# Kernel optimization log

Measured on AMD Instinct MI355X. Metric: run time of the kernel, lower is better.

## Reference

```python
import jax, jax.numpy as jnp
import numpy as np

HEADS = 4

def _rope(Q, K):
    # Q, K: [B, T, H, F]; split last dim into 4 chunks of w = F // 4
    w = Q.shape[-1] // 4
    T = Q.shape[-3]
    Q1r, Q1i, Q2r, Q2i = jnp.split(Q, 4, axis=-1)
    K1r, K1i, K2r, K2i = jnp.split(K, 4, axis=-1)
    Pt = jnp.arange(T, dtype=Q.dtype).reshape(1, -1, 1, 1)
    Df = (2.0 ** (-jnp.arange(w, dtype=Q.dtype))).reshape(1, 1, 1, -1)
    U = Pt * Df / 16.0
    Ur, Ui = jnp.sin(U), jnp.cos(U)  # names match the original (sin first)
    rot = lambda r, i: (r * Ur - i * Ui, r * Ui + i * Ur)
    Q1r, Q1i = rot(Q1r, Q1i)
    Q2r, Q2i = rot(Q2r, Q2i)
    K1r, K1i = rot(K1r, K1i)
    K2r, K2i = rot(K2r, K2i)
    return (jnp.concatenate([Q1r, Q1i], -1), jnp.concatenate([Q2r, Q2i], -1),
            jnp.concatenate([K1r, K1i], -1), jnp.concatenate([K2r, K2i], -1))


def setup_inputs() -> dict:
    key = jax.random.key(0)
    ks = jax.random.split(key, 8)
    B, F, T = 4, 512, 2048
    sd = 1.0 / np.sqrt(F)
    return {
        "x": jax.random.normal(ks[0], (B, F, T), jnp.float32),
        "Wq": jax.random.normal(ks[1], (F, F), jnp.float32) * sd,
        "bq": jax.random.normal(ks[2], (F,), jnp.float32) * sd,
        "Wk": jax.random.normal(ks[3], (F, F), jnp.float32) * sd,
        "bk": jax.random.normal(ks[4], (F,), jnp.float32) * sd,
        "Wv": jax.random.normal(ks[5], (F, F), jnp.float32) * sd,
        "bv": jax.random.normal(ks[6], (F,), jnp.float32) * sd,
        "s2": jax.random.uniform(ks[7], (HEADS,), jnp.float32),
    }


def reference(x, Wq, bq, Wk, bk, Wv, bv, s2):
    # x: [B, feat, T] -> transpose to [B, T, feat]; cond defaults to x
    B, F, T = x.shape
    H = HEADS
    hf = F // H
    scale = jnp.asarray(np.sqrt(F // 2), x.dtype)
    xt = jnp.swapaxes(x, -1, -2)  # [B, T, F]
    Q = (xt @ Wq.T + bq).reshape(B, T, H, hf)
    K = (xt @ Wk.T + bk).reshape(B, T, H, hf)
    V = (xt @ Wv.T + bv).reshape(B, T, H, hf)
    Q1, Q2, K1, K2 = _rope(Q, K)
    A1 = jax.nn.softmax(jnp.einsum('bqhf,bkhf->bhqk', Q1, K1) / scale, axis=-1)
    A2 = jax.nn.softmax(jnp.einsum('bqhf,bkhf->bhqk', Q2, K2) / scale, axis=-1)
    A = A1 - A2 * s2[None, :, None, None]
    R = jnp.einsum('bhqk,bkhf->bqhf', A, V)
    y = R.reshape(B, T, F)
    return jnp.swapaxes(xt + y, -1, -2)  # [B, feat, T]
```

## Files before the change

### kernel.cpp

```cpp
#include <hip/hip_runtime.h>
#include <math.h>

#define B_DIM 4
#define F_DIM 512
#define T_DIM 2048
#define H_DIM 4
#define HF    128

typedef __attribute__((ext_vector_type(8))) short short8;
typedef __attribute__((ext_vector_type(4))) float floatx4;

__device__ __forceinline__ unsigned short f2bf(float f) {
    return (unsigned short)((__float_as_uint(f) + 0x8000u) >> 16);
}

__device__ __forceinline__ unsigned pkbf2(float a, float b) {
    const unsigned ua = __float_as_uint(a) + 0x8000u;
    const unsigned ub = __float_as_uint(b) + 0x8000u;
    return __builtin_amdgcn_perm(ub, ua, 0x07060302u);
}

__device__ __forceinline__ short8 pack8(const float* v) {
    union { unsigned u[4]; short8 s; } r;
    #pragma unroll
    for (int j = 0; j < 4; ++j) r.u[j] = pkbf2(v[2*j], v[2*j+1]);
    return r.s;
}

__device__ __forceinline__ void gload16(const unsigned short* g, unsigned short* l) {
    __builtin_amdgcn_global_load_lds(
        (const __attribute__((address_space(1))) void*)g,
        (__attribute__((address_space(3))) void*)l, 16, 0, 0);
}

__global__ __launch_bounds__(256)
void prep_kernel(const float* __restrict__ x,
                 const float* __restrict__ Wq, const float* __restrict__ Wk,
                 const float* __restrict__ Wv,
                 unsigned short* __restrict__ xt,
                 unsigned short* __restrict__ Wqb, unsigned short* __restrict__ Wkb,
                 unsigned short* __restrict__ Wvb)
{
    const int tid = threadIdx.x;
    if (blockIdx.z < B_DIM) {
        const int b  = blockIdx.z;
        const int t0 = blockIdx.x * 64;
        const int f0 = blockIdx.y * 64;
        __shared__ float Ls[64][67];
        const float* __restrict__ xb = x + (size_t)b * F_DIM * T_DIM;
        #pragma unroll
        for (int it = 0; it < 4; ++it) {
            const int fr = (tid >> 4) + 16 * it;
            const int tc = (tid & 15) << 2;
            const float4 v = *(const float4*)(xb + (size_t)(f0 + fr) * T_DIM + t0 + tc);
            Ls[fr][tc+0] = v.x; Ls[fr][tc+1] = v.y; Ls[fr][tc+2] = v.z; Ls[fr][tc+3] = v.w;
        }
        __syncthreads();
        const int f8 = tid & 7;
        const int tb = tid >> 3;
        #pragma unroll
        for (int it2 = 0; it2 < 2; ++it2) {
            const int t = tb + 32 * it2;
            float v[8];
            #pragma unroll
            for (int j = 0; j < 8; ++j) v[j] = Ls[8*f8 + j][t];
            *(short8*)(xt + ((size_t)b * T_DIM + t0 + t) * F_DIM + f0 + 8*f8) = pack8(v);
        }
    } else {
        const int blockId = blockIdx.y * 32 + blockIdx.x;
        const int g0 = blockId * 256 + tid;
        const int perW = F_DIM * F_DIM / 8;
        for (int chunk = g0; chunk < 3 * perW; chunk += 65536) {
            const int wsel = chunk / perW;
            const int rem  = chunk - wsel * perW;
            const float* __restrict__ Ws = (wsel == 0) ? Wq : (wsel == 1) ? Wk : Wv;
            unsigned short* __restrict__ Wd = (wsel == 0) ? Wqb : (wsel == 1) ? Wkb : Wvb;
            float v[8];
            *(float4*)&v[0] = *(const float4*)(Ws + (size_t)rem * 8);
            *(float4*)&v[4] = *(const float4*)(Ws + (size_t)rem * 8 + 4);
            *(short8*)(Wd + (size_t)rem * 8) = pack8(v);
        }
    }
}

#define ASTR 136

__global__ __launch_bounds__(256, 3)
void proj_kernel(const unsigned short* __restrict__ xt,
                 const unsigned short* __restrict__ Wqb,
                 const unsigned short* __restrict__ Wkb,
                 const unsigned short* __restrict__ Wvb,
                 const float* __restrict__ bq, const float* __restrict__ bk,
                 const float* __restrict__ bv,
                 unsigned short* __restrict__ Qb, unsigned short* __restrict__ Kb,
                 unsigned short* __restrict__ Vtb)
{
    __shared__ unsigned short As[128][ASTR];
    __shared__ unsigned short Bs[64][ASTR];

    const int tid  = threadIdx.x;
    const int w    = tid >> 6;
    const int lane = tid & 63;
    const int ln15 = lane & 15;
    const int quad = lane >> 4;

    const bool is_v = (blockIdx.z >= 8);
    int t0, fo0, b;
    const unsigned short *Asrc, *Bsrc;
    if (!is_v) {
        t0  = blockIdx.x * 128;
        fo0 = blockIdx.y * 64;
        b   = blockIdx.z >> 1;
        Asrc = xt + (size_t)b * T_DIM * F_DIM + (size_t)t0 * F_DIM;
        Bsrc = ((blockIdx.z & 1) ? Wkb : Wqb) + (size_t)fo0 * F_DIM;
    } else {
        const int idx = blockIdx.y * 16 + blockIdx.x;
        fo0 = (idx >> 5) * 128;
        t0  = (idx & 31) * 64;
        b   = blockIdx.z - 8;
        Asrc = Wvb + (size_t)fo0 * F_DIM;
        Bsrc = xt + (size_t)b * T_DIM * F_DIM + (size_t)t0 * F_DIM;
    }

    floatx4 acc[2][4];
    #pragma unroll
    for (int mi = 0; mi < 2; ++mi)
        #pragma unroll
        for (int nt = 0; nt < 4; ++nt) acc[mi][nt] = (floatx4){0.f,0.f,0.f,0.f};

    for (int f0 = 0; f0 < F_DIM; f0 += 128) {
        __syncthreads();
        #pragma unroll
        for (int it = 0; it < 8; ++it) {
            const int idx = tid + it * 256;
            const int r = idx >> 4, c = (idx & 15) * 8;
            *(short8*)&As[r][c] = *(const short8*)(Asrc + (size_t)r * F_DIM + f0 + c);
        }
        #pragma unroll
        for (int it = 0; it < 4; ++it) {
            const int idx = tid + it * 256;
            const int r = idx >> 4, c = (idx & 15) * 8;
            *(short8*)&Bs[r][c] = *(const short8*)(Bsrc + (size_t)r * F_DIM + f0 + c);
        }
        __syncthreads();
        #pragma unroll
        for (int ks = 0; ks < 4; ++ks) {
            short8 a[2], bb[4];
            a[0] = *(const short8*)&As[w*32      + ln15][ks*32 + quad*8];
            a[1] = *(const short8*)&As[w*32 + 16 + ln15][ks*32 + quad*8];
            #pragma unroll
            for (int nt = 0; nt < 4; ++nt)
                bb[nt] = *(const short8*)&Bs[16*nt + ln15][ks*32 + quad*8];
            #pragma unroll
            for (int mi = 0; mi < 2; ++mi)
                #pragma unroll
                for (int nt = 0; nt < 4; ++nt)
                    acc[mi][nt] = __builtin_amdgcn_mfma_f32_16x16x32_bf16(
                        a[mi], bb[nt], acc[mi][nt], 0, 0, 0);
        }
    }

    if (!is_v) {
        const int which = blockIdx.z & 1;
        const float* bias = which ? bk : bq;
        unsigned short* __restrict__ Out =
            (which ? Kb : Qb) + (size_t)b * T_DIM * F_DIM;
        const float oscale = which ? 1.0f : 0.0625f * 1.4426950408889634f;
        float bn[4];
        #pragma unroll
        for (int nt = 0; nt < 4; ++nt) bn[nt] = bias[fo0 + 16*nt + ln15];
        const float pw[2] = {
            __uint_as_float((unsigned)(123 - ln15) << 23),
            __uint_as_float((unsigned)(107 - ln15) << 23)
        };
        #pragma unroll
        for (int mi = 0; mi < 2; ++mi) {
            #pragma unroll
            for (int r = 0; r < 4; ++r) {
                const int t = t0 + w*32 + 16*mi + quad*4 + r;
                unsigned short* rowp = Out + (size_t)t * F_DIM + fo0;
                #pragma unroll
                for (int pr = 0; pr < 2; ++pr) {
                    const int wi = 16*pr + ln15;
                    const float re = acc[mi][pr  ][r] + bn[pr];
                    const float im = acc[mi][pr+2][r] + bn[pr+2];
                    const float u = (float)t * pw[pr];
                    float sn, cs;
                    __sincosf(u, &sn, &cs);
                    rowp[wi]      = f2bf((re * sn - im * cs) * oscale);
                    rowp[wi + 32] = f2bf((re * cs + im * sn) * oscale);
                }
            }
        }
    } else {
        #pragma unroll
        for (int mi = 0; mi < 2; ++mi) {
            #pragma unroll
            for (int r = 0; r < 4; ++r) {
                const int fo = fo0 + w*32 + 16*mi + quad*4 + r;
                const float bvv = bv[fo];
                unsigned short* rowp = Vtb + ((size_t)b * F_DIM + fo) * T_DIM + t0;
                #pragma unroll
                for (int nt = 0; nt < 4; ++nt)
                    rowp[16*nt + ln15] = f2bf(acc[mi][nt][r] + bvv);
            }
        }
    }
}

__global__ __launch_bounds__(512, 2)
void attn_kernel(const unsigned short* __restrict__ Qb,
                 const unsigned short* __restrict__ Kb,
                 const unsigned short* __restrict__ Vtb,
                 const float* __restrict__ x,
                 const float* __restrict__ s2g,
                 float* __restrict__ out)
{
    __shared__ unsigned short smem[2][2][16384];

    const int tid  = threadIdx.x;
    const int w8   = tid >> 6;
    const int half = w8 >> 2;
    const int qg   = w8 & 3;
    const int lane = tid & 63;
    const int ln15 = lane & 15;
    const int quad = lane >> 4;

    const int flat = blockIdx.x + 16 * (blockIdx.y + 4 * blockIdx.z);
    const int swz  = (flat & 7) * 32 + (flat >> 3);
    const int q0 = (swz & 15) * 128;
    const int h  = (swz >> 4) & 3;
    const int b  = swz >> 6;

    const int kbase = half << 10;

    const unsigned short* __restrict__ Qg =
        Qb + ((size_t)b * T_DIM + q0 + qg * 32) * F_DIM + h * HF;
    const unsigned short* __restrict__ Kg =
        Kb + (size_t)b * T_DIM * F_DIM + h * HF;
    const unsigned short* __restrict__ Vg =
        Vtb + ((size_t)b * F_DIM + h * HF) * T_DIM;

    int koff[4], voff[4];
    #pragma unroll
    for (int it = 0; it < 4; ++it) {
        const int m = qg * 4 + it;
        {
            const int rd = 4 * m + (lane >> 4);
            const int r  = (rd & 32) | ((rd & 12) << 1) | ((rd & 16) >> 2) | (rd & 3);
            const int c  = (lane & 15) ^ (rd & 15);
            koff[it] = r * F_DIM + c * 8;
        }
        {
            const int rd = 8 * m + (lane >> 3);
            const int c  = (lane & 7) ^ (rd & 7);
            voff[it] = rd * T_DIM + c * 8;
        }
    }

    auto stage = [&](int buf, int k) {
        unsigned short* Kd = &smem[half][buf][0]    + qg * 2048;
        unsigned short* Vd = &smem[half][buf][8192] + qg * 2048;
        const unsigned short* Kp = Kg + (size_t)(kbase + k) * F_DIM;
        const unsigned short* Vp = Vg + (kbase + k);
        #pragma unroll
        for (int it = 0; it < 4; ++it) {
            gload16(Kp + koff[it], Kd + it * 512);
            gload16(Vp + voff[it], Vd + it * 512);
        }
    };

    short8 qa[2][4];
    #pragma unroll
    for (int g = 0; g < 2; ++g)
        #pragma unroll
        for (int c = 0; c < 4; ++c)
            qa[g][c] = *(const short8*)(Qg + (size_t)(g * 16 + ln15) * F_DIM + quad * 8 + 32 * c);

    floatx4 O1t[2][8], O2t[2][8];
    #pragma unroll
    for (int g = 0; g < 2; ++g)
        #pragma unroll
        for (int ft = 0; ft < 8; ++ft) {
            O1t[g][ft] = (floatx4){0.f, 0.f, 0.f, 0.f};
            O2t[g][ft] = (floatx4){0.f, 0.f, 0.f, 0.f};
        }
    float l1[2] = {0.f, 0.f}, l2[2] = {0.f, 0.f};

    stage(0, 0);

    for (int k0 = 0; k0 < 1024; k0 += 64) {
        asm volatile("s_waitcnt vmcnt(0)" ::: "memory");
        __syncthreads();
        const int buf = (k0 >> 6) & 1;
        if (k0 + 64 < 1024) stage(buf ^ 1, k0 + 64);

        const unsigned short* Ks = &smem[half][buf][0];
        const unsigned short* Vs = &smem[half][buf][8192];

        short8 p1f[2][2], p2f[2][2];
        #pragma unroll
        for (int tp = 0; tp < 2; ++tp) {
            float e1[2][8], e2[2][8];
            #pragma unroll
            for (int tt = 0; tt < 2; ++tt) {
                const int t = tp * 2 + tt;
                const unsigned short* krow = &Ks[(16 * t + ln15) * 128];
                const short8 k0f = *(const short8*)(krow + ((quad     ) ^ ln15) * 8);
                const short8 k1f = *(const short8*)(krow + ((quad +  4) ^ ln15) * 8);
                const short8 k2f = *(const short8*)(krow + ((quad +  8) ^ ln15) * 8);
                const short8 k3f = *(const short8*)(krow + ((quad + 12) ^ ln15) * 8);
                #pragma unroll
                for (int g = 0; g < 2; ++g) {
                    floatx4 z = (floatx4){0.f, 0.f, 0.f, 0.f};
                    floatx4 s = __builtin_amdgcn_mfma_f32_16x16x32_bf16(k0f, qa[g][0], z, 0, 0, 0);
                    s         = __builtin_amdgcn_mfma_f32_16x16x32_bf16(k1f, qa[g][1], s, 0, 0, 0);
                    floatx4 u = __builtin_amdgcn_mfma_f32_16x16x32_bf16(k2f, qa[g][2], z, 0, 0, 0);
                    u         = __builtin_amdgcn_mfma_f32_16x16x32_bf16(k3f, qa[g][3], u, 0, 0, 0);
                    #pragma unroll
                    for (int r = 0; r < 4; ++r) {
                        e1[g][tt*4 + r] = __builtin_amdgcn_exp2f(s[r]);
                        e2[g][tt*4 + r] = __builtin_amdgcn_exp2f(u[r]);
                    }
                }
            }
            #pragma unroll
            for (int g = 0; g < 2; ++g) {
                #pragma unroll
                for (int j = 0; j < 8; ++j) { l1[g] += e1[g][j]; l2[g] += e2[g][j]; }
                p1f[g][tp] = pack8(&e1[g][0]);
                p2f[g][tp] = pack8(&e2[g][0]);
            }
        }

        #pragma unroll
        for (int p = 0; p < 2; ++p) {
            #pragma unroll
            for (int ft = 0; ft < 8; ++ft) {
                const short8 va = *(const short8*)
                    (&Vs[(16*ft + ln15) * 64 + (((4*p + quad) ^ (ln15 & 7))) * 8]);
                O1t[0][ft] = __builtin_amdgcn_mfma_f32_16x16x32_bf16(va, p1f[0][p], O1t[0][ft], 0, 0, 0);
                O1t[1][ft] = __builtin_amdgcn_mfma_f32_16x16x32_bf16(va, p1f[1][p], O1t[1][ft], 0, 0, 0);
                O2t[0][ft] = __builtin_amdgcn_mfma_f32_16x16x32_bf16(va, p2f[0][p], O2t[0][ft], 0, 0, 0);
                O2t[1][ft] = __builtin_amdgcn_mfma_f32_16x16x32_bf16(va, p2f[1][p], O2t[1][ft], 0, 0, 0);
            }
        }
    }

    #pragma unroll
    for (int g = 0; g < 2; ++g) {
        l1[g] += __shfl_xor(l1[g], 16); l1[g] += __shfl_xor(l1[g], 32);
        l2[g] += __shfl_xor(l2[g], 16); l2[g] += __shfl_xor(l2[g], 32);
    }

    float* comb = (float*)&smem[0][0][0];
    __syncthreads();
    if (half == 1) {
        if (quad == 0) {
            #pragma unroll
            for (int g = 0; g < 2; ++g) {
                comb[      qg*32 + g*16 + ln15] = l1[g];
                comb[128 + qg*32 + g*16 + ln15] = l2[g];
            }
        }
        #pragma unroll
        for (int g = 0; g < 2; ++g)
            #pragma unroll
            for (int ft = 0; ft < 8; ++ft)
                #pragma unroll
                for (int r = 0; r < 4; ++r)
                    comb[512 + (((g*8 + ft)*4 + r) * 256) + qg*64 + lane] = O1t[g][ft][r];
    }
    __syncthreads();
    if (half == 0) {
        #pragma unroll
        for (int g = 0; g < 2; ++g) {
            l1[g] += comb[      qg*32 + g*16 + ln15];
            l2[g] += comb[128 + qg*32 + g*16 + ln15];
        }
        #pragma unroll
        for (int g = 0; g < 2; ++g)
            #pragma unroll
            for (int ft = 0; ft < 8; ++ft)
                #pragma unroll
                for (int r = 0; r < 4; ++r)
                    O1t[g][ft][r] += comb[512 + (((g*8 + ft)*4 + r) * 256) + qg*64 + lane];
    }
    __syncthreads();
    if (half == 1) {
        #pragma unroll
        for (int g = 0; g < 2; ++g)
            #pragma unroll
            for (int ft = 0; ft < 8; ++ft)
                #pragma unroll
                for (int r = 0; r < 4; ++r)
                    comb[512 + (((g*8 + ft)*4 + r) * 256) + qg*64 + lane] = O2t[g][ft][r];
    }
    __syncthreads();
    if (half == 0) {
        #pragma unroll
        for (int g = 0; g < 2; ++g)
            #pragma unroll
            for (int ft = 0; ft < 8; ++ft)
                #pragma unroll
                for (int r = 0; r < 4; ++r)
                    O2t[g][ft][r] += comb[512 + (((g*8 + ft)*4 + r) * 256) + qg*64 + lane];

        const float s2h = s2g[h];
        float i1[2], i2[2];
        #pragma unroll
        for (int g = 0; g < 2; ++g) { i1[g] = 1.f / l1[g]; i2[g] = s2h / l2[g]; }
        const size_t obase = (size_t)b * F_DIM * T_DIM;
        const int f0 = h * HF;
        #pragma unroll
        for (int g = 0; g < 2; ++g) {
            const int t = q0 + qg*32 + g*16 + ln15;
            #pragma unroll
            for (int ft = 0; ft < 8; ++ft) {
                #pragma unroll
                for (int r = 0; r < 4; ++r) {
                    const int feat = 16*ft + 4*quad + r;
                    const size_t idx = obase + (size_t)(f0 + feat) * T_DIM + t;
                    out[idx] = x[idx] + O1t[g][ft][r] * i1[g] - O2t[g][ft][r] * i2[g];
                }
            }
        }
    }
}

extern "C" void kernel_launch(void* const* d_in, const int* in_sizes, int n_in,
                              void* d_out, int out_size, void* d_ws, size_t ws_size,
                              hipStream_t stream)
{
    const float* x  = (const float*)d_in[0];
    const float* Wq = (const float*)d_in[1];
    const float* bq = (const float*)d_in[2];
    const float* Wk = (const float*)d_in[3];
    const float* bk = (const float*)d_in[4];
    const float* Wv = (const float*)d_in[5];
    const float* bv = (const float*)d_in[6];
    const float* s2 = (const float*)d_in[7];
    float* out = (float*)d_out;

    const size_t per = (size_t)B_DIM * T_DIM * F_DIM;
    const size_t wsz = (size_t)F_DIM * F_DIM;
    unsigned short* xt  = (unsigned short*)d_ws;
    unsigned short* Wqb = xt + per;
    unsigned short* Wkb = Wqb + wsz;
    unsigned short* Wvb = Wkb + wsz;
    unsigned short* Qb  = Wvb + wsz;
    unsigned short* Kb  = Qb + per;
    unsigned short* Vtb = Kb + per;

    hipLaunchKernelGGL(prep_kernel, dim3(32, 8, 5), dim3(256), 0, stream,
                       x, Wq, Wk, Wv, xt, Wqb, Wkb, Wvb);

    hipLaunchKernelGGL(proj_kernel, dim3(16, 8, 12), dim3(256), 0, stream,
                       xt, Wqb, Wkb, Wvb, bq, bk, bv, Qb, Kb, Vtb);

    hipLaunchKernelGGL(attn_kernel, dim3(16, 4, 4), dim3(512), 0, stream,
                       Qb, Kb, Vtb, x, s2, out);
}
```

Measured before the change: 93.31 us.

## Software-pipeline attention inner loop: interleave exp with PV MFMAs, add setprio

Restructures the attention main loop. The outer loop is unrolled by two so buffer offsets become compile-time constants, and LDS pointers are precomputed per lane. The QK MFMAs for the second key half and the exp/pack work are interleaved with the PV MFMAs so transcendental VALU work overlaps matrix work. s_setprio raises wave priority around the MFMA bursts. The interleaving adds register pressure from holding more score tiles live, which could reduce occupancy or cause spills.

```diff
diff --git a/kernel.cpp b/kernel.cpp
--- a/kernel.cpp
+++ b/kernel.cpp
@@ -258,92 +258,183 @@
         }
     }
 
-    auto stage = [&](int buf, int k) {
-        unsigned short* Kd = &smem[half][buf][0]    + qg * 2048;
-        unsigned short* Vd = &smem[half][buf][8192] + qg * 2048;
-        const unsigned short* Kp = Kg + (size_t)(kbase + k) * F_DIM;
-        const unsigned short* Vp = Vg + (kbase + k);
+    const unsigned short* kp[4];
+    #pragma unroll
+    for (int j = 0; j < 4; ++j)
+        kp[j] = &smem[half][0][0] + ln15 * 128 + ((quad + 4*j) ^ ln15) * 8;
+    const unsigned short* vp[2];
+    #pragma unroll
+    for (int p = 0; p < 2; ++p)
+        vp[p] = &smem[half][0][8192] + ln15 * 64 + (((4*p + quad) ^ (ln15 & 7))) * 8;
+
+    short8 qa[2][4];
+    #pragma unroll
+    for (int g = 0; g < 2; ++g)
+        #pragma unroll
+        for (int c = 0; c < 4; ++c)
+            qa[g][c] = *(const short8*)(Qg + (size_t)(g * 16 + ln15) * F_DIM + quad * 8 + 32 * c);
+
+    floatx4 O1t[2][8], O2t[2][8];
+    #pragma unroll
+    for (int g = 0; g < 2; ++g)
+        #pragma unroll
+        for (int ft = 0; ft < 8; ++ft) {
+            O1t[g][ft] = (floatx4){0.f, 0.f, 0.f, 0.f};
+            O2t[g][ft] = (floatx4){0.f, 0.f, 0.f, 0.f};
+        }
+    float l1[2] = {0.f, 0.f}, l2[2] = {0.f, 0.f};
+
+    {
+        unsigned short* Kd = &smem[half][0][0]    + qg * 2048;
+        unsigned short* Vd = &smem[half][0][8192] + qg * 2048;
+        const unsigned short* Kp = Kg + (size_t)kbase * F_DIM;
+        const unsigned short* Vp = Vg + kbase;
         #pragma unroll
         for (int it = 0; it < 4; ++it) {
             gload16(Kp + koff[it], Kd + it * 512);
             gload16(Vp + voff[it], Vd + it * 512);
         }
-    };
-
-    short8 qa[2][4];
-    #pragma unroll
-    for (int g = 0; g < 2; ++g)
-        #pragma unroll
-        for (int c = 0; c < 4; ++c)
-            qa[g][c] = *(const short8*)(Qg + (size_t)(g * 16 + ln15) * F_DIM + quad * 8 + 32 * c);
-
-    floatx4 O1t[2][8], O2t[2][8];
-    #pragma unroll
-    for (int g = 0; g < 2; ++g)
-        #pragma unroll
-        for (int ft = 0; ft < 8; ++ft) {
-            O1t[g][ft] = (floatx4){0.f, 0.f, 0.f, 0.f};
-            O2t[g][ft] = (floatx4){0.f, 0.f, 0.f, 0.f};
-        }
-    float l1[2] = {0.f, 0.f}, l2[2] = {0.f, 0.f};
-
-    stage(0, 0);
-
-    for (int k0 = 0; k0 < 1024; k0 += 64) {
-        asm volatile("s_waitcnt vmcnt(0)" ::: "memory");
-        __syncthreads();
-        const int buf = (k0 >> 6) & 1;
-        if (k0 + 64 < 1024) stage(buf ^ 1, k0 + 64);
-
-        const unsigned short* Ks = &smem[half][buf][0];
-        const unsigned short* Vs = &smem[half][buf][8192];
-
-        short8 p1f[2][2], p2f[2][2];
-        #pragma unroll
-        for (int tp = 0; tp < 2; ++tp) {
-            float e1[2][8], e2[2][8];
+    }
+
+    for (int k0o = 0; k0o < 1024; k0o += 128) {
+        #pragma unroll
+        for (int sub = 0; sub < 2; ++sub) {
+            const int k0 = k0o + sub * 64;
+            asm volatile("s_waitcnt vmcnt(0)" ::: "memory");
+            __syncthreads();
+
+            if (k0 + 64 < 1024) {
+                unsigned short* Kd = &smem[half][sub ^ 1][0]    + qg * 2048;
+                unsigned short* Vd = &smem[half][sub ^ 1][8192] + qg * 2048;
+                const unsigned short* Kp = Kg + (size_t)(kbase + k0 + 64) * F_DIM;
+                const unsigned short* Vp = Vg + (kbase + k0 + 64);
+                #pragma unroll
+                for (int it = 0; it < 4; ++it) {
+                    gload16(Kp + koff[it], Kd + it * 512);
+                    gload16(Vp + voff[it], Vd + it * 512);
+                }
+            }
+
+            const int BO = sub * 16384;
+
+            floatx4 sA[2][2], uA[2][2];
+            __builtin_amdgcn_s_setprio(1);
             #pragma unroll
             for (int tt = 0; tt < 2; ++tt) {
-                const int t = tp * 2 + tt;
-                const unsigned short* krow = &Ks[(16 * t + ln15) * 128];
-                const short8 k0f = *(const short8*)(krow + ((quad     ) ^ ln15) * 8);
-                const short8 k1f = *(const short8*)(krow + ((quad +  4) ^ ln15) * 8);
-                const short8 k2f = *(const short8*)(krow + ((quad +  8) ^ ln15) * 8);
-                const short8 k3f = *(const short8*)(krow + ((quad + 12) ^ ln15) * 8);
+                const short8 k0f = *(const short8*)(kp[0] + BO + tt * 2048);
+                const short8 k1f = *(const short8*)(kp[1] + BO + tt * 2048);
+                const short8 k2f = *(const short8*)(kp[2] + BO + tt * 2048);
+                const short8 k3f = *(const short8*)(kp[3] + BO + tt * 2048);
                 #pragma unroll
                 for (int g = 0; g < 2; ++g) {
                     floatx4 z = (floatx4){0.f, 0.f, 0.f, 0.f};
                     floatx4 s = __builtin_amdgcn_mfma_f32_16x16x32_bf16(k0f, qa[g][0], z, 0, 0, 0);
-                    s         = __builtin_amdgcn_mfma_f32_16x16x32_bf16(k1f, qa[g][1], s, 0, 0, 0);
+                    sA[g][tt] = __builtin_amdgcn_mfma_f32_16x16x32_bf16(k1f, qa[g][1], s, 0, 0, 0);
                     floatx4 u = __builtin_amdgcn_mfma_f32_16x16x32_bf16(k2f, qa[g][2], z, 0, 0, 0);
-                    u         = __builtin_amdgcn_mfma_f32_16x16x32_bf16(k3f, qa[g][3], u, 0, 0, 0);
+                    uA[g][tt] = __builtin_amdgcn_mfma_f32_16x16x32_bf16(k3f, qa[g][3], u, 0, 0, 0);
+                }
+            }
+            __builtin_amdgcn_s_setprio(0);
+
+            short8 p1a[2], p2a[2];
+            #pragma unroll
+            for (int g = 0; g < 2; ++g) {
+                float e1[8], e2[8];
+                #pragma unroll
+                for (int tt = 0; tt < 2; ++tt)
                     #pragma unroll
                     for (int r = 0; r < 4; ++r) {
-                        e1[g][tt*4 + r] = __builtin_amdgcn_exp2f(s[r]);
-                        e2[g][tt*4 + r] = __builtin_amdgcn_exp2f(u[r]);
+                        e1[tt*4 + r] = __builtin_amdgcn_exp2f(sA[g][tt][r]);
+                        e2[tt*4 + r] = __builtin_amdgcn_exp2f(uA[g][tt][r]);
                     }
+                #pragma unroll
+                for (int j = 0; j < 8; ++j) { l1[g] += e1[j]; l2[g] += e2[j]; }
+                p1a[g] = pack8(e1);
+                p2a[g] = pack8(e2);
+            }
+
+            floatx4 sB[2][2], uB[2][2];
+            __builtin_amdgcn_s_setprio(1);
+            #pragma unroll
+            for (int tt = 0; tt < 2; ++tt) {
+                const short8 k0f = *(const short8*)(kp[0] + BO + (2 + tt) * 2048);
+                const short8 k1f = *(const short8*)(kp[1] + BO + (2 + tt) * 2048);
+                const short8 k2f = *(const short8*)(kp[2] + BO + (2 + tt) * 2048);
+                const short8 k3f = *(const short8*)(kp[3] + BO + (2 + tt) * 2048);
+                #pragma unroll
+                for (int g = 0; g < 2; ++g) {
+                    floatx4 z = (floatx4){0.f, 0.f, 0.f, 0.f};
+                    floatx4 s = __builtin_amdgcn_mfma_f32_16x16x32_bf16(k0f, qa[g][0], z, 0, 0, 0);
+                    sB[g][tt] = __builtin_amdgcn_mfma_f32_16x16x32_bf16(k1f, qa[g][1], s, 0, 0, 0);
+                    floatx4 u = __builtin_amdgcn_mfma_f32_16x16x32_bf16(k2f, qa[g][2], z, 0, 0, 0);
+                    uB[g][tt] = __builtin_amdgcn_mfma_f32_16x16x32_bf16(k3f, qa[g][3], u, 0, 0, 0);
                 }
             }
-            #pragma unroll
-            for (int g = 0; g < 2; ++g) {
-                #pragma unroll
-                for (int j = 0; j < 8; ++j) { l1[g] += e1[g][j]; l2[g] += e2[g][j]; }
-                p1f[g][tp] = pack8(&e1[g][0]);
-                p2f[g][tp] = pack8(&e2[g][0]);
-            }
-        }
-
-        #pragma unroll
-        for (int p = 0; p < 2; ++p) {
+            __builtin_amdgcn_s_setprio(0);
+
+            __builtin_amdgcn_s_setprio(1);
+            #pragma unroll
+            for (int ft = 0; ft < 4; ++ft) {
+                const short8 va = *(const short8*)(vp[0] + BO + ft * 1024);
+                O1t[0][ft] = __builtin_amdgcn_mfma_f32_16x16x32_bf16(va, p1a[0], O1t[0][ft], 0, 0, 0);
+                O1t[1][ft] = __builtin_amdgcn_mfma_f32_16x16x32_bf16(va, p1a[1], O1t[1][ft], 0, 0, 0);
+                O2t[0][ft] = __builtin_amdgcn_mfma_f32_16x16x32_bf16(va, p2a[0], O2t[0][ft], 0, 0, 0);
+                O2t[1][ft] = __builtin_amdgcn_mfma_f32_16x16x32_bf16(va, p2a[1], O2t[1][ft], 0, 0, 0);
+            }
+            __builtin_amdgcn_s_setprio(0);
+
+            short8 p1b[2], p2b[2];
+            {
+                float e1[8], e2[8];
+                #pragma unroll
+                for (int tt = 0; tt < 2; ++tt)
+                    #pragma unroll
+                    for (int r = 0; r < 4; ++r) {
+                        e1[tt*4 + r] = __builtin_amdgcn_exp2f(sB[0][tt][r]);
+                        e2[tt*4 + r] = __builtin_amdgcn_exp2f(uB[0][tt][r]);
+                    }
+                #pragma unroll
+                for (int j = 0; j < 8; ++j) { l1[0] += e1[j]; l2[0] += e2[j]; }
+                p1b[0] = pack8(e1);
+                p2b[0] = pack8(e2);
+            }
+
+            __builtin_amdgcn_s_setprio(1);
+            #pragma unroll
+            for (int ft = 4; ft < 8; ++ft) {
+                const short8 va = *(const short8*)(vp[0] + BO + ft * 1024);
+                O1t[0][ft] = __builtin_amdgcn_mfma_f32_16x16x32_bf16(va, p1a[0], O1t[0][ft], 0, 0, 0);
+                O1t[1][ft] = __builtin_amdgcn_mfma_f32_16x16x32_bf16(va, p1a[1], O1t[1][ft], 0, 0, 0);
+                O2t[0][ft] = __builtin_amdgcn_mfma_f32_16x16x32_bf16(va, p2a[0], O2t[0][ft], 0, 0, 0);
+                O2t[1][ft] = __builtin_amdgcn_mfma_f32_16x16x32_bf16(va, p2a[1], O2t[1][ft], 0, 0, 0);
+            }
+            __builtin_amdgcn_s_setprio(0);
+
+            {
+                float e1[8], e2[8];
+                #pragma unroll
+                for (int tt = 0; tt < 2; ++tt)
+                    #pragma unroll
+                    for (int r = 0; r < 4; ++r) {
+                        e1[tt*4 + r] = __builtin_amdgcn_exp2f(sB[1][tt][r]);
+                        e2[tt*4 + r] = __builtin_amdgcn_exp2f(uB[1][tt][r]);
+                    }
+                #pragma unroll
+                for (int j = 0; j < 8; ++j) { l1[1] += e1[j]; l2[1] += e2[j]; }
+                p1b[1] = pack8(e1);
+                p2b[1] = pack8(e2);
+            }
+
+            __builtin_amdgcn_s_setprio(1);
             #pragma unroll
             for (int ft = 0; ft < 8; ++ft) {
-                const short8 va = *(const short8*)
-                    (&Vs[(16*ft + ln15) * 64 + (((4*p + quad) ^ (ln15 & 7))) * 8]);
-                O1t[0][ft] = __builtin_amdgcn_mfma_f32_16x16x32_bf16(va, p1f[0][p], O1t[0][ft], 0, 0, 0);
-                O1t[1][ft] = __builtin_amdgcn_mfma_f32_16x16x32_bf16(va, p1f[1][p], O1t[1][ft], 0, 0, 0);
-                O2t[0][ft] = __builtin_amdgcn_mfma_f32_16x16x32_bf16(va, p2f[0][p], O2t[0][ft], 0, 0, 0);
-                O2t[1][ft] = __builtin_amdgcn_mfma_f32_16x16x32_bf16(va, p2f[1][p], O2t[1][ft], 0, 0, 0);
-            }
+                const short8 va = *(const short8*)(vp[1] + BO + ft * 1024);
+                O1t[0][ft] = __builtin_amdgcn_mfma_f32_16x16x32_bf16(va, p1b[0], O1t[0][ft], 0, 0, 0);
+                O1t[1][ft] = __builtin_amdgcn_mfma_f32_16x16x32_bf16(va, p1b[1], O1t[1][ft], 0, 0, 0);
+                O2t[0][ft] = __builtin_amdgcn_mfma_f32_16x16x32_bf16(va, p2b[0], O2t[0][ft], 0, 0, 0);
+                O2t[1][ft] = __builtin_amdgcn_mfma_f32_16x16x32_bf16(va, p2b[1], O2t[1][ft], 0, 0, 0);
+            }
+            __builtin_amdgcn_s_setprio(0);
         }
     }
 
```

Result: slower. 172.9 us (+85.3%).

## Drop split-K across wave halves in attention kernel; loop full key range per block

Applied to the files above, without the earlier changes.

The attention kernel previously used 512 threads, with two halves of 4 waves each processing half of the key range and then combining partial sums and outputs through shared memory. It now uses 256 threads, with each wave walking all 2048 keys, so the LDS reduction and its four barriers go away. The loop is also unrolled by two so the buffer index is static, and s_setprio raises wave priority around the PV MFMA block. The cost is half as many waves per block, and each wave runs a key loop twice as long, which reduces latency hiding over a grid of only 256 blocks.

```diff
diff --git a/kernel.cpp b/kernel.cpp
--- a/kernel.cpp
+++ b/kernel.cpp
@@ -208,7 +208,7 @@
     }
 }
 
-__global__ __launch_bounds__(512, 2)
+__global__ __launch_bounds__(256, 2)
 void attn_kernel(const unsigned short* __restrict__ Qb,
                  const unsigned short* __restrict__ Kb,
                  const unsigned short* __restrict__ Vtb,
@@ -216,12 +216,10 @@
                  const float* __restrict__ s2g,
                  float* __restrict__ out)
 {
-    __shared__ unsigned short smem[2][2][16384];
+    __shared__ unsigned short smem[2][16384];
 
     const int tid  = threadIdx.x;
-    const int w8   = tid >> 6;
-    const int half = w8 >> 2;
-    const int qg   = w8 & 3;
+    const int qg   = tid >> 6;
     const int lane = tid & 63;
     const int ln15 = lane & 15;
     const int quad = lane >> 4;
@@ -231,8 +229,6 @@
     const int q0 = (swz & 15) * 128;
     const int h  = (swz >> 4) & 3;
     const int b  = swz >> 6;
-
-    const int kbase = half << 10;
 
     const unsigned short* __restrict__ Qg =
         Qb + ((size_t)b * T_DIM + q0 + qg * 32) * F_DIM + h * HF;
@@ -259,10 +255,10 @@
     }
 
     auto stage = [&](int buf, int k) {
-        unsigned short* Kd = &smem[half][buf][0]    + qg * 2048;
-        unsigned short* Vd = &smem[half][buf][8192] + qg * 2048;
-        const unsigned short* Kp = Kg + (size_t)(kbase + k) * F_DIM;
-        const unsigned short* Vp = Vg + (kbase + k);
+        unsigned short* Kd = &smem[buf][0]    + qg * 2048;
+        unsigned short* Vd = &smem[buf][8192] + qg * 2048;
+        const unsigned short* Kp = Kg + (size_t)k * F_DIM;
+        const unsigned short* Vp = Vg + k;
         #pragma unroll
         for (int it = 0; it < 4; ++it) {
             gload16(Kp + koff[it], Kd + it * 512);
@@ -289,61 +285,66 @@
 
     stage(0, 0);
 
-    for (int k0 = 0; k0 < 1024; k0 += 64) {
-        asm volatile("s_waitcnt vmcnt(0)" ::: "memory");
-        __syncthreads();
-        const int buf = (k0 >> 6) & 1;
-        if (k0 + 64 < 1024) stage(buf ^ 1, k0 + 64);
-
-        const unsigned short* Ks = &smem[half][buf][0];
-        const unsigned short* Vs = &smem[half][buf][8192];
-
-        short8 p1f[2][2], p2f[2][2];
-        #pragma unroll
-        for (int tp = 0; tp < 2; ++tp) {
-            float e1[2][8], e2[2][8];
-            #pragma unroll
-            for (int tt = 0; tt < 2; ++tt) {
-                const int t = tp * 2 + tt;
-                const unsigned short* krow = &Ks[(16 * t + ln15) * 128];
-                const short8 k0f = *(const short8*)(krow + ((quad     ) ^ ln15) * 8);
-                const short8 k1f = *(const short8*)(krow + ((quad +  4) ^ ln15) * 8);
-                const short8 k2f = *(const short8*)(krow + ((quad +  8) ^ ln15) * 8);
-                const short8 k3f = *(const short8*)(krow + ((quad + 12) ^ ln15) * 8);
-                #pragma unroll
-                for (int g = 0; g < 2; ++g) {
-                    floatx4 z = (floatx4){0.f, 0.f, 0.f, 0.f};
-                    floatx4 s = __builtin_amdgcn_mfma_f32_16x16x32_bf16(k0f, qa[g][0], z, 0, 0, 0);
-                    s         = __builtin_amdgcn_mfma_f32_16x16x32_bf16(k1f, qa[g][1], s, 0, 0, 0);
-                    floatx4 u = __builtin_amdgcn_mfma_f32_16x16x32_bf16(k2f, qa[g][2], z, 0, 0, 0);
-                    u         = __builtin_amdgcn_mfma_f32_16x16x32_bf16(k3f, qa[g][3], u, 0, 0, 0);
+    for (int k0o = 0; k0o < 2048; k0o += 128) {
+        #pragma unroll
+        for (int sub = 0; sub < 2; ++sub) {
+            const int k0 = k0o + sub * 64;
+            asm volatile("s_waitcnt vmcnt(0)" ::: "memory");
+            __syncthreads();
+            if (k0 + 64 < 2048) stage(sub ^ 1, k0 + 64);
+
+            const unsigned short* Ks = &smem[sub][0];
+            const unsigned short* Vs = &smem[sub][8192];
+
+            short8 p1f[2][2], p2f[2][2];
+            #pragma unroll
+            for (int tp = 0; tp < 2; ++tp) {
+                float e1[2][8], e2[2][8];
+                #pragma unroll
+                for (int tt = 0; tt < 2; ++tt) {
+                    const int t = tp * 2 + tt;
+                    const unsigned short* krow = &Ks[(16 * t + ln15) * 128];
+                    const short8 k0f = *(const short8*)(krow + ((quad     ) ^ ln15) * 8);
+                    const short8 k1f = *(const short8*)(krow + ((quad +  4) ^ ln15) * 8);
+                    const short8 k2f = *(const short8*)(krow + ((quad +  8) ^ ln15) * 8);
+                    const short8 k3f = *(const short8*)(krow + ((quad + 12) ^ ln15) * 8);
                     #pragma unroll
-                    for (int r = 0; r < 4; ++r) {
-                        e1[g][tt*4 + r] = __builtin_amdgcn_exp2f(s[r]);
-                        e2[g][tt*4 + r] = __builtin_amdgcn_exp2f(u[r]);
+                    for (int g = 0; g < 2; ++g) {
+                        floatx4 z = (floatx4){0.f, 0.f, 0.f, 0.f};
+                        floatx4 s = __builtin_amdgcn_mfma_f32_16x16x32_bf16(k0f, qa[g][0], z, 0, 0, 0);
+                        s         = __builtin_amdgcn_mfma_f32_16x16x32_bf16(k1f, qa[g][1], s, 0, 0, 0);
+                        floatx4 u = __builtin_amdgcn_mfma_f32_16x16x32_bf16(k2f, qa[g][2], z, 0, 0, 0);
+                        u         = __builtin_amdgcn_mfma_f32_16x16x32_bf16(k3f, qa[g][3], u, 0, 0, 0);
+                        #pragma unroll
+                        for (int r = 0; r < 4; ++r) {
+                            e1[g][tt*4 + r] = __builtin_amdgcn_exp2f(s[r]);
+                            e2[g][tt*4 + r] = __builtin_amdgcn_exp2f(u[r]);
+                        }
                     }
                 }
+                #pragma unroll
+                for (int g = 0; g < 2; ++g) {
+                    #pragma unroll
+                    for (int j = 0; j < 8; ++j) { l1[g] += e1[g][j]; l2[g] += e2[g][j]; }
+                    p1f[g][tp] = pack8(&e1[g][0]);
+                    p2f[g][tp] = pack8(&e2[g][0]);
+                }
             }
-            #pragma unroll
-            for (int g = 0; g < 2; ++g) {
-                #pragma unroll
-                for (int j = 0; j < 8; ++j) { l1[g] += e1[g][j]; l2[g] += e2[g][j]; }
-                p1f[g][tp] = pack8(&e1[g][0]);
-                p2f[g][tp] = pack8(&e2[g][0]);
+
+            __builtin_amdgcn_s_setprio(1);
+            #pragma unroll
+            for (int p = 0; p < 2; ++p) {
+                #pragma unroll
+                for (int ft = 0; ft < 8; ++ft) {
+                    const short8 va = *(const short8*)
+                        (&Vs[(16*ft + ln15) * 64 + (((4*p + quad) ^ (ln15 & 7))) * 8]);
+                    O1t[0][ft] = __builtin_amdgcn_mfma_f32_16x16x32_bf16(va, p1f[0][p], O1t[0][ft], 0, 0, 0);
+                    O1t[1][ft] = __builtin_amdgcn_mfma_f32_16x16x32_bf16(va, p1f[1][p], O1t[1][ft], 0, 0, 0);
+                    O2t[0][ft] = __builtin_amdgcn_mfma_f32_16x16x32_bf16(va, p2f[0][p], O2t[0][ft], 0, 0, 0);
+                    O2t[1][ft] = __builtin_amdgcn_mfma_f32_16x16x32_bf16(va, p2f[1][p], O2t[1][ft], 0, 0, 0);
+                }
             }
-        }
-
-        #pragma unroll
-        for (int p = 0; p < 2; ++p) {
-            #pragma unroll
-            for (int ft = 0; ft < 8; ++ft) {
-                const short8 va = *(const short8*)
-                    (&Vs[(16*ft + ln15) * 64 + (((4*p + quad) ^ (ln15 & 7))) * 8]);
-                O1t[0][ft] = __builtin_amdgcn_mfma_f32_16x16x32_bf16(va, p1f[0][p], O1t[0][ft], 0, 0, 0);
-                O1t[1][ft] = __builtin_amdgcn_mfma_f32_16x16x32_bf16(va, p1f[1][p], O1t[1][ft], 0, 0, 0);
-                O2t[0][ft] = __builtin_amdgcn_mfma_f32_16x16x32_bf16(va, p2f[0][p], O2t[0][ft], 0, 0, 0);
-                O2t[1][ft] = __builtin_amdgcn_mfma_f32_16x16x32_bf16(va, p2f[1][p], O2t[1][ft], 0, 0, 0);
-            }
+            __builtin_amdgcn_s_setprio(0);
         }
     }
 
@@ -353,76 +354,22 @@
         l2[g] += __shfl_xor(l2[g], 16); l2[g] += __shfl_xor(l2[g], 32);
     }
 
-    float* comb = (float*)&smem[0][0][0];
-    __syncthreads();
-    if (half == 1) {
-        if (quad == 0) {
-            #pragma unroll
-            for (int g = 0; g < 2; ++g) {
-                comb[      qg*32 + g*16 + ln15] = l1[g];
-                comb[128 + qg*32 + g*16 + ln15] = l2[g];
-            }
-        }
-        #pragma unroll
-        for (int g = 0; g < 2; ++g)
-            #pragma unroll
-            for (int ft = 0; ft < 8; ++ft)
-                #pragma unroll
-                for (int r = 0; r < 4; ++r)
-                    comb[512 + (((g*8 + ft)*4 + r) * 256) + qg*64 + lane] = O1t[g][ft][r];
-    }
-    __syncthreads();
-    if (half == 0) {
-        #pragma unroll
-        for (int g = 0; g < 2; ++g) {
-            l1[g] += comb[      qg*32 + g*16 + ln15];
-            l2[g] += comb[128 + qg*32 + g*16 + ln15];
-        }
-        #pragma unroll
-        for (int g = 0; g < 2; ++g)
-            #pragma unroll
-            for (int ft = 0; ft < 8; ++ft)
-                #pragma unroll
-                for (int r = 0; r < 4; ++r)
-                    O1t[g][ft][r] += comb[512 + (((g*8 + ft)*4 + r) * 256) + qg*64 + lane];
-    }
-    __syncthreads();
-    if (half == 1) {
-        #pragma unroll
-        for (int g = 0; g < 2; ++g)
-            #pragma unroll
-            for (int ft = 0; ft < 8; ++ft)
-                #pragma unroll
-                for (int r = 0; r < 4; ++r)
-                    comb[512 + (((g*8 + ft)*4 + r) * 256) + qg*64 + lane] = O2t[g][ft][r];
-    }
-    __syncthreads();
-    if (half == 0) {
-        #pragma unroll
-        for (int g = 0; g < 2; ++g)
-            #pragma unroll
-            for (int ft = 0; ft < 8; ++ft)
-                #pragma unroll
-                for (int r = 0; r < 4; ++r)
-                    O2t[g][ft][r] += comb[512 + (((g*8 + ft)*4 + r) * 256) + qg*64 + lane];
-
-        const float s2h = s2g[h];
-        float i1[2], i2[2];
-        #pragma unroll
-        for (int g = 0; g < 2; ++g) { i1[g] = 1.f / l1[g]; i2[g] = s2h / l2[g]; }
-        const size_t obase = (size_t)b * F_DIM * T_DIM;
-        const int f0 = h * HF;
-        #pragma unroll
-        for (int g = 0; g < 2; ++g) {
-            const int t = q0 + qg*32 + g*16 + ln15;
-            #pragma unroll
-            for (int ft = 0; ft < 8; ++ft) {
-                #pragma unroll
-                for (int r = 0; r < 4; ++r) {
-                    const int feat = 16*ft + 4*quad + r;
-                    const size_t idx = obase + (size_t)(f0 + feat) * T_DIM + t;
-                    out[idx] = x[idx] + O1t[g][ft][r] * i1[g] - O2t[g][ft][r] * i2[g];
-                }
+    const float s2h = s2g[h];
+    float i1[2], i2[2];
+    #pragma unroll
+    for (int g = 0; g < 2; ++g) { i1[g] = 1.f / l1[g]; i2[g] = s2h / l2[g]; }
+    const size_t obase = (size_t)b * F_DIM * T_DIM;
+    const int f0 = h * HF;
+    #pragma unroll
+    for (int g = 0; g < 2; ++g) {
+        const int t = q0 + qg*32 + g*16 + ln15;
+        #pragma unroll
+        for (int ft = 0; ft < 8; ++ft) {
+            #pragma unroll
+            for (int r = 0; r < 4; ++r) {
+                const int feat = 16*ft + 4*quad + r;
+                const size_t idx = obase + (size_t)(f0 + feat) * T_DIM + t;
+                out[idx] = x[idx] + O1t[g][ft][r] * i1[g] - O2t[g][ft][r] * i2[g];
             }
         }
     }
@@ -458,6 +405,6 @@
     hipLaunchKernelGGL(proj_kernel, dim3(16, 8, 12), dim3(256), 0, stream,
                        xt, Wqb, Wkb, Wvb, bq, bk, bv, Qb, Kb, Vtb);
 
-    hipLaunchKernelGGL(attn_kernel, dim3(16, 4, 4), dim3(512), 0, stream,
+    hipLaunchKernelGGL(attn_kernel, dim3(16, 4, 4), dim3(256), 0, stream,
                        Qb, Kb, Vtb, x, s2, out);
 }
```

New measurement: 185.9 us. +99.3%, slower.
